# Kernel tuning notes

Hardware: AMD Instinct MI355X
Metric: run time of the kernel (lower is better)

Reference implementation:

```python
import jax, jax.numpy as jnp
import numpy as np

HIDDEN = 2048
HEADS = 16
HEAD_DIM = HIDDEN // HEADS
LATENT = 512
B, T = 2, 2048


def setup_inputs() -> dict:
    key = jax.random.key(0)
    ks = jax.random.split(key, 12)
    s = lambda fan_in: 1.0 / np.sqrt(fan_in)
    x = jax.random.normal(ks[0], (B, T, HIDDEN), dtype=jnp.float32)
    Wq = jax.random.uniform(ks[1], (HIDDEN, HIDDEN), jnp.float32, -s(HIDDEN), s(HIDDEN))
    bq = jax.random.uniform(ks[2], (HIDDEN,), jnp.float32, -s(HIDDEN), s(HIDDEN))
    Wl = jax.random.uniform(ks[3], (HIDDEN, LATENT), jnp.float32, -s(HIDDEN), s(HIDDEN))
    bl = jax.random.uniform(ks[4], (LATENT,), jnp.float32, -s(HIDDEN), s(HIDDEN))
    # per-head back-projections stacked along head axis: [H, latent, head_dim]
    Wk = jax.random.uniform(ks[5], (HEADS, LATENT, HEAD_DIM), jnp.float32, -s(LATENT), s(LATENT))
    bk = jax.random.uniform(ks[6], (HEADS, HEAD_DIM), jnp.float32, -s(LATENT), s(LATENT))
    Wv = jax.random.uniform(ks[7], (HEADS, LATENT, HEAD_DIM), jnp.float32, -s(LATENT), s(LATENT))
    bv = jax.random.uniform(ks[8], (HEADS, HEAD_DIM), jnp.float32, -s(LATENT), s(LATENT))
    Wo = jax.random.uniform(ks[9], (HIDDEN, HIDDEN), jnp.float32, -s(HIDDEN), s(HIDDEN))
    bo = jax.random.uniform(ks[10], (HIDDEN,), jnp.float32, -s(HIDDEN), s(HIDDEN))
    return {"x": x, "Wq": Wq, "bq": bq, "Wl": Wl, "bl": bl,
            "Wk": Wk, "bk": bk, "Wv": Wv, "bv": bv, "Wo": Wo, "bo": bo}


def reference(x, Wq, bq, Wl, bl, Wk, bk, Wv, bv, Wo, bo):
    Bc, Tc, _ = x.shape
    # Q projection, split into heads: [B, H, T, Dh]
    q = (x @ Wq + bq).reshape(Bc, Tc, HEADS, HEAD_DIM).transpose(0, 2, 1, 3)
    # shared low-rank latent KV (cache=None -> just new tokens): [B, T, L]
    latent = x @ Wl + bl
    # per-head back-projections fused as one grouped matmul: [B, H, T, Dh]
    k = jnp.einsum('btl,hld->bhtd', latent, Wk) + bk[None, :, None, :]
    v = jnp.einsum('btl,hld->bhtd', latent, Wv) + bv[None, :, None, :]
    # full (non-causal) attention, matching the original module
    scores = jnp.einsum('bhqd,bhkd->bhqk', q, k) / np.sqrt(HEAD_DIM).astype(jnp.float32)
    probs = jax.nn.softmax(scores, axis=-1)
    attn = jnp.einsum('bhqk,bhkd->bhqd', probs, v)
    attn = attn.transpose(0, 2, 1, 3).reshape(Bc, Tc, HIDDEN)
    return attn @ Wo + bo
```

## Files before the change

kernel.cpp:

```cpp
#include <hip/hip_runtime.h>
#include <hip/hip_bf16.h>
#include <cstdint>

#define SEQ     2048
#define NHID    2048
#define NLAT    512
#define NHEAD   16
#define DHEAD   128
#define NBATCH  2
#define NROWS   (NBATCH*SEQ)

typedef unsigned short u16;
typedef __attribute__((ext_vector_type(8))) short short8;
typedef __attribute__((ext_vector_type(4))) float f32x4;

#define MFMA16 __builtin_amdgcn_mfma_f32_16x16x32_bf16

#define QSCALE 0.12751743f

#if __has_builtin(__builtin_amdgcn_exp2f)
#define EXP2(x) __builtin_amdgcn_exp2f(x)
#else
#define EXP2(x) __expf((x) * 0.6931471805599453f)
#endif

__device__ __forceinline__ u16 f2b(float f) {
    uint32_t u = __float_as_uint(f);
    uint32_t r = (u + 0x7fffu + ((u >> 16) & 1u)) >> 16;
    return (u16)r;
}

__device__ __forceinline__ uint32_t cvt_pk_bf16(float a, float b) {
    uint32_t r;
    asm("v_cvt_pk_bf16_f32 %0, %1, %2" : "=v"(r) : "v"(a), "v"(b));
    return r;
}

__device__ __forceinline__ void async16(const u16* g, u16* l) {
    __builtin_amdgcn_global_load_lds(
        (const __attribute__((address_space(1))) unsigned int*)g,
        (__attribute__((address_space(3))) unsigned int*)l, 16, 0, 0);
}

__device__ __forceinline__ void stage_lds(const u16* __restrict__ src, size_t strideE,
                                          u16* lds, int wave, int lane,
                                          int log2cpr, int xmask, int xshift,
                                          int reps, int nlanes) {
    const int cmask = (1 << log2cpr) - 1;
    for (int rep = 0; rep < reps; ++rep) {
        int cbase = rep * nlanes + wave * 64;
        int ci = cbase + lane;
        int row = ci >> log2cpr;
        int sc = ci & cmask;
        int dchunk = sc ^ ((row >> xshift) & xmask);
        const u16* g = src + (size_t)row * strideE + dchunk * 8;
        async16(g, lds + (size_t)cbase * 8);
    }
}

__global__ __launch_bounds__(256) void prep(const float* __restrict__ x,
                                            const float* __restrict__ Wq,
                                            const float* __restrict__ Wl,
                                            const float* __restrict__ Wk,
                                            const float* __restrict__ Wv,
                                            const float* __restrict__ Wo,
                                            u16* __restrict__ xb,
                                            u16* __restrict__ WqlT,
                                            u16* __restrict__ WkvT,
                                            u16* __restrict__ WoT) {
    const int t = blockIdx.x, tid = threadIdx.x;
    if (t < 8192) {
        int i = t * 256 + tid;
        float4 v = ((const float4*)x)[i];
        unsigned int lo = (unsigned int)f2b(v.x) | ((unsigned int)f2b(v.y) << 16);
        unsigned int hi = (unsigned int)f2b(v.z) | ((unsigned int)f2b(v.w) << 16);
        ((uint2*)xb)[i] = make_uint2(lo, hi);
        return;
    }
    __shared__ float tile[32][33];
    const float* src; u16* dst; int R, C, tY, tX;
    if (t < 12288)      { int tt = t - 8192;  src = Wq; dst = WqlT;           R = 2048; C = 2048; tY = tt >> 6; tX = tt & 63; }
    else if (t < 13312) { int tt = t - 12288; src = Wl; dst = WqlT + 4194304; R = 2048; C = 512;  tY = tt >> 4; tX = tt & 15; }
    else if (t < 14336) { int tt = t - 13312; int hh = tt >> 6; tt &= 63;
                          src = Wk + hh * 65536; dst = WkvT + hh * 65536;     R = 512;  C = 128;  tY = tt >> 2; tX = tt & 3; }
    else if (t < 15360) { int tt = t - 14336; int hh = tt >> 6; tt &= 63;
                          src = Wv + hh * 65536; dst = WkvT + 1048576 + hh * 65536;
                                                                              R = 512;  C = 128;  tY = tt >> 2; tX = tt & 3; }
    else                { int tt = t - 15360; src = Wo; dst = WoT;            R = 2048; C = 2048; tY = tt >> 6; tX = tt & 63; }
    const int tx = tid & 31, ty = tid >> 5;
    const int r0 = tY * 32, c0 = tX * 32;
    #pragma unroll
    for (int i = 0; i < 32; i += 8)
        tile[ty + i][tx] = src[(size_t)(r0 + ty + i) * C + c0 + tx];
    __syncthreads();
    #pragma unroll
    for (int i = 0; i < 32; i += 8)
        dst[(size_t)(c0 + ty + i) * R + r0 + tx] = f2b(tile[tx][ty + i]);
}

template<int STORE>
__global__ __launch_bounds__(256) void gemm_bt(const u16* __restrict__ A,
                                               const u16* __restrict__ Bt,
                                               const float* __restrict__ bias1,
                                               const float* __restrict__ bias2,
                                               void* __restrict__ C1,
                                               void* __restrict__ C2,
                                               int M, int N, int K) {
    __shared__ __align__(16) u16 As[2][128 * 32];
    __shared__ __align__(16) u16 Bs[2][128 * 32];
    const int tid = threadIdx.x, wave = tid >> 6, lane = tid & 63;
    const int quad = lane >> 4, m16 = lane & 15;
    const int m0 = blockIdx.y * 128, n0 = blockIdx.x * 128;
    const int wr = wave >> 1, wc = wave & 1;
    const int swz = (quad ^ ((m16 >> 1) & 3)) * 8;
    const u16* Ab = A + (size_t)m0 * K;
    const u16* Bb = Bt + (size_t)n0 * K;
    const int KI = K >> 5;

    stage_lds(Ab, K, As[0], wave, lane, 2, 3, 1, 2, 256);
    stage_lds(Bb, K, Bs[0], wave, lane, 2, 3, 1, 2, 256);

    f32x4 acc[4][4] = {};
    for (int it = 0; it < KI; ++it) {
        const int cur = it & 1;
        __syncthreads();
        if (it + 1 < KI) {
            stage_lds(Ab + (it + 1) * 32, K, As[cur ^ 1], wave, lane, 2, 3, 1, 2, 256);
            stage_lds(Bb + (it + 1) * 32, K, Bs[cur ^ 1], wave, lane, 2, 3, 1, 2, 256);
        }
        short8 af[4], bfr[4];
        #pragma unroll
        for (int i = 0; i < 4; i++)
            af[i] = *(const short8*)&As[cur][(wr * 64 + i * 16 + m16) * 32 + swz];
        #pragma unroll
        for (int j = 0; j < 4; j++)
            bfr[j] = *(const short8*)&Bs[cur][(wc * 64 + j * 16 + m16) * 32 + swz];
        #pragma unroll
        for (int i = 0; i < 4; i++)
            #pragma unroll
            for (int j = 0; j < 4; j++)
                acc[i][j] = MFMA16(af[i], bfr[j], acc[i][j], 0, 0, 0);
    }
    const bool second = (n0 >= 2048);
    #pragma unroll
    for (int j = 0; j < 4; j++) {
        int n = n0 + wc * 64 + j * 16 + m16;
        float bv;
        if constexpr (STORE == 2) bv = bias1[n];
        else bv = second ? bias2[n - 2048] : bias1[n];
        #pragma unroll
        for (int i = 0; i < 4; i++) {
            int mrow = m0 + wr * 64 + i * 16 + quad * 4;
            if constexpr (STORE == 4) {
                if (second) {
                    int n2 = n - 2048;
                    ushort4 pk;
                    pk.x = f2b(acc[i][j][0] + bv);
                    pk.y = f2b(acc[i][j][1] + bv);
                    pk.z = f2b(acc[i][j][2] + bv);
                    pk.w = f2b(acc[i][j][3] + bv);
                    *(ushort4*)&((u16*)C2)[((size_t)((m0 >> 11) * 2048 + n2)) * 2048 +
                                           (mrow & 2047)] = pk;
                    continue;
                }
            }
            #pragma unroll
            for (int r = 0; r < 4; r++) {
                float v = acc[i][j][r] + bv;
                int m = mrow + r;
                if constexpr (STORE == 2)
                    ((float*)C1)[(size_t)m * N + n] = v;
                else if constexpr (STORE == 3) {
                    if (!second) ((u16*)C1)[(size_t)m * 2048 + n] = f2b(v * QSCALE);
                    else         ((u16*)C2)[(size_t)m * 512 + (n - 2048)] = f2b(v);
                } else {
                    ((u16*)C1)[(size_t)m * 2048 + n] = f2b(v);
                }
            }
        }
    }
}

__global__ __launch_bounds__(256, 2) void attn_fused(const u16* __restrict__ Q,
                                                     const u16* __restrict__ Kf,
                                                     const u16* __restrict__ Vt,
                                                     u16* __restrict__ Ob) {
    __shared__ __align__(16) u16 Kt[2][64 * 128];
    __shared__ __align__(16) u16 Vtile[2][128 * 64];
    __shared__ __align__(16) u16 Ps[4][32 * 64];
    const int tid = threadIdx.x, wave = tid >> 6, lane = tid & 63;
    const int quad = lane >> 4, m16 = lane & 15;
    const int bh = blockIdx.y, b = bh >> 4, h = bh & 15;
    const int q0 = blockIdx.x * 128;
    const size_t grow = (size_t)b * SEQ;
    const u16* Kbase = Kf + grow * NHID + h * DHEAD;
    const u16* Vbase = Vt + (grow + h * DHEAD) * SEQ;

    const u16* qsrc = Q + (grow + q0) * NHID + h * DHEAD;
    stage_lds(qsrc, NHID, Kt[0], wave, lane, 4, 15, 0, 4, 256);
    stage_lds(qsrc + (size_t)64 * NHID, NHID, Kt[1], wave, lane, 4, 15, 0, 4, 256);
    __syncthreads();
    short8 qf[2][4];
    {
        const u16* qbuf = Kt[wave >> 1];
        int rbase = (wave & 1) * 32;
        #pragma unroll
        for (int i = 0; i < 2; i++)
            #pragma unroll
            for (int c = 0; c < 4; c++)
                qf[i][c] = *(const short8*)&qbuf[(rbase + i * 16 + m16) * 128 +
                                                (((c * 4 + quad) ^ m16)) * 8];
    }
    __syncthreads();

    stage_lds(Kbase, NHID, Kt[0], wave, lane, 4, 15, 0, 4, 256);
    stage_lds(Vbase, SEQ, Vtile[0], wave, lane, 3, 7, 0, 4, 256);

    f32x4 o[2][8] = {};
    float lsum[2][4] = {};

    for (int it = 0; it < SEQ / 64; ++it) {
        const int cur = it & 1;
        __syncthreads();
        if (it + 1 < SEQ / 64) {
            stage_lds(Kbase + (size_t)(it + 1) * 64 * NHID, NHID, Kt[cur ^ 1],
                      wave, lane, 4, 15, 0, 4, 256);
            stage_lds(Vbase + (it + 1) * 64, SEQ, Vtile[cur ^ 1],
                      wave, lane, 3, 7, 0, 4, 256);
        }
        const u16* kt = Kt[cur];
        const u16* vt = Vtile[cur];

        f32x4 s[2][4] = {};
        __builtin_amdgcn_s_setprio(1);
        #pragma unroll
        for (int c = 0; c < 4; c++)
            #pragma unroll
            for (int j = 0; j < 4; j++) {
                short8 kb = *(const short8*)&kt[(j * 16 + m16) * 128 +
                                               (((c * 4 + quad) ^ m16)) * 8];
                s[0][j] = MFMA16(qf[0][c], kb, s[0][j], 0, 0, 0);
                s[1][j] = MFMA16(qf[1][c], kb, s[1][j], 0, 0, 0);
            }
        __builtin_amdgcn_s_setprio(0);

        u16* pw = Ps[wave];
        #pragma unroll
        for (int i = 0; i < 2; i++)
            #pragma unroll
            for (int r = 0; r < 4; r++) {
                int rowl = i * 16 + quad * 4 + r;
                float p0 = EXP2(s[i][0][r]);
                float p1 = EXP2(s[i][1][r]);
                float p2 = EXP2(s[i][2][r]);
                float p3 = EXP2(s[i][3][r]);
                lsum[i][r] += (p0 + p1) + (p2 + p3);
                uint32_t pk01 = cvt_pk_bf16(p0, p1);
                uint32_t pk23 = cvt_pk_bf16(p2, p3);
                const int x = rowl & 7;
                u16* base = pw + rowl * 64 + (m16 & 7);
                const int hb = m16 >> 3;
                base[((0 + hb) ^ x) * 8] = (u16)pk01;
                base[((2 + hb) ^ x) * 8] = (u16)(pk01 >> 16);
                base[((4 + hb) ^ x) * 8] = (u16)pk23;
                base[((6 + hb) ^ x) * 8] = (u16)(pk23 >> 16);
            }

        __builtin_amdgcn_s_setprio(1);
        #pragma unroll
        for (int c2 = 0; c2 < 2; c2++) {
            short8 pa[2];
            #pragma unroll
            for (int i = 0; i < 2; i++)
                pa[i] = *(const short8*)&pw[(i * 16 + m16) * 64 +
                                            (((c2 * 4 + quad) ^ (m16 & 7))) * 8];
            #pragma unroll
            for (int jd = 0; jd < 8; jd++) {
                short8 vb = *(const short8*)&vt[(jd * 16 + m16) * 64 +
                                               (((c2 * 4 + quad) ^ (m16 & 7))) * 8];
                o[0][jd] = MFMA16(pa[0], vb, o[0][jd], 0, 0, 0);
                o[1][jd] = MFMA16(pa[1], vb, o[1][jd], 0, 0, 0);
            }
        }
        __builtin_amdgcn_s_setprio(0);
    }

    #pragma unroll
    for (int i = 0; i < 2; i++) {
        float inv[4];
        #pragma unroll
        for (int r = 0; r < 4; r++) {
            float v = lsum[i][r];
            #pragma unroll
            for (int off = 1; off < 16; off <<= 1)
                v += __shfl_xor(v, off);
            inv[r] = 1.f / v;
        }
        #pragma unroll
        for (int jd = 0; jd < 8; jd++)
            #pragma unroll
            for (int r = 0; r < 4; r++) {
                int t = q0 + wave * 32 + i * 16 + quad * 4 + r;
                int d = jd * 16 + m16;
                Ob[(grow + t) * NHID + h * DHEAD + d] = f2b(o[i][jd][r] * inv[r]);
            }
    }
}

extern "C" void kernel_launch(void* const* d_in, const int* in_sizes, int n_in,
                              void* d_out, int out_size, void* d_ws, size_t ws_size,
                              hipStream_t stream) {
    const float* x  = (const float*)d_in[0];
    const float* Wq = (const float*)d_in[1];
    const float* bq = (const float*)d_in[2];
    const float* Wl = (const float*)d_in[3];
    const float* bl = (const float*)d_in[4];
    const float* Wk = (const float*)d_in[5];
    const float* bk = (const float*)d_in[6];
    const float* Wv = (const float*)d_in[7];
    const float* bv = (const float*)d_in[8];
    const float* Wo = (const float*)d_in[9];
    const float* bo = (const float*)d_in[10];
    float* out = (float*)d_out;

    u16* w = (u16*)d_ws;
    u16* xb    = w;
    u16* WqlT  = xb    + 8388608;
    u16* WkvT  = WqlT  + 5242880;
    u16* WoT   = WkvT  + 2097152;
    u16* qb    = WoT   + 4194304;
    u16* kb    = qb    + 8388608;
    u16* vt    = kb    + 8388608;
    u16* lat   = vt    + 8388608;
    u16* attnb = xb;

    prep<<<19456, 256, 0, stream>>>(x, Wq, Wl, Wk, Wv, Wo, xb, WqlT, WkvT, WoT);

    gemm_bt<3><<<dim3(20, 32), 256, 0, stream>>>(xb, WqlT, bq, bl, qb, lat,
                                                 NROWS, 2560, 2048);
    gemm_bt<4><<<dim3(32, 32), 256, 0, stream>>>(lat, WkvT, bk, bv, kb, vt,
                                                 NROWS, 4096, 512);

    attn_fused<<<dim3(16, 32), 256, 0, stream>>>(qb, kb, vt, attnb);

    gemm_bt<2><<<dim3(16, 32), 256, 0, stream>>>(attnb, WoT, bo, nullptr, out, nullptr,
                                                 NROWS, 2048, 2048);
}
```

Measured before the change: 343.9 us.

## Keep softmax probabilities in registers via transposed QK MFMA and permlane swaps

Swaps the MFMA operand order for QK^T so each lane holds score columns for one query row. The bf16 probabilities can then be assembled into PV A-operands with permlane32 swaps instead of a round-trip through LDS. To make the k-index order match, the V-transpose store in the projection GEMM permutes bits 2 and 3 of the sequence index. This removes the per-wave P shared-memory buffer and its stores, loads and bank traffic, and simplifies the row-sum reduction, at the cost of a coupled layout change across two kernels.

```diff
diff --git a/kernel.cpp b/kernel.cpp
--- a/kernel.cpp
+++ b/kernel.cpp
@@ -154,13 +154,14 @@
             if constexpr (STORE == 4) {
                 if (second) {
                     int n2 = n - 2048;
-                    ushort4 pk;
-                    pk.x = f2b(acc[i][j][0] + bv);
-                    pk.y = f2b(acc[i][j][1] + bv);
-                    pk.z = f2b(acc[i][j][2] + bv);
-                    pk.w = f2b(acc[i][j][3] + bv);
-                    *(ushort4*)&((u16*)C2)[((size_t)((m0 >> 11) * 2048 + n2)) * 2048 +
-                                           (mrow & 2047)] = pk;
+                    ushort4 pkv;
+                    pkv.x = f2b(acc[i][j][0] + bv);
+                    pkv.y = f2b(acc[i][j][1] + bv);
+                    pkv.z = f2b(acc[i][j][2] + bv);
+                    pkv.w = f2b(acc[i][j][3] + bv);
+                    int c = mrow & 2047;
+                    c = (c & ~12) | ((c & 4) << 1) | ((c & 8) >> 1);
+                    *(ushort4*)&((u16*)C2)[((size_t)((m0 >> 11) * 2048 + n2)) * 2048 + c] = pkv;
                     continue;
                 }
             }
@@ -187,7 +188,6 @@
                                                      u16* __restrict__ Ob) {
     __shared__ __align__(16) u16 Kt[2][64 * 128];
     __shared__ __align__(16) u16 Vtile[2][128 * 64];
-    __shared__ __align__(16) u16 Ps[4][32 * 64];
     const int tid = threadIdx.x, wave = tid >> 6, lane = tid & 63;
     const int quad = lane >> 4, m16 = lane & 15;
     const int bh = blockIdx.y, b = bh >> 4, h = bh & 15;
@@ -217,7 +217,7 @@
     stage_lds(Vbase, SEQ, Vtile[0], wave, lane, 3, 7, 0, 4, 256);
 
     f32x4 o[2][8] = {};
-    float lsum[2][4] = {};
+    float lsum[2] = {};
 
     for (int it = 0; it < SEQ / 64; ++it) {
         const int cur = it & 1;
@@ -239,41 +239,56 @@
             for (int j = 0; j < 4; j++) {
                 short8 kb = *(const short8*)&kt[(j * 16 + m16) * 128 +
                                                (((c * 4 + quad) ^ m16)) * 8];
-                s[0][j] = MFMA16(qf[0][c], kb, s[0][j], 0, 0, 0);
-                s[1][j] = MFMA16(qf[1][c], kb, s[1][j], 0, 0, 0);
+                s[0][j] = MFMA16(kb, qf[0][c], s[0][j], 0, 0, 0);
+                s[1][j] = MFMA16(kb, qf[1][c], s[1][j], 0, 0, 0);
             }
         __builtin_amdgcn_s_setprio(0);
 
-        u16* pw = Ps[wave];
-        #pragma unroll
-        for (int i = 0; i < 2; i++)
-            #pragma unroll
-            for (int r = 0; r < 4; r++) {
-                int rowl = i * 16 + quad * 4 + r;
-                float p0 = EXP2(s[i][0][r]);
-                float p1 = EXP2(s[i][1][r]);
-                float p2 = EXP2(s[i][2][r]);
-                float p3 = EXP2(s[i][3][r]);
-                lsum[i][r] += (p0 + p1) + (p2 + p3);
-                uint32_t pk01 = cvt_pk_bf16(p0, p1);
-                uint32_t pk23 = cvt_pk_bf16(p2, p3);
-                const int x = rowl & 7;
-                u16* base = pw + rowl * 64 + (m16 & 7);
-                const int hb = m16 >> 3;
-                base[((0 + hb) ^ x) * 8] = (u16)pk01;
-                base[((2 + hb) ^ x) * 8] = (u16)(pk01 >> 16);
-                base[((4 + hb) ^ x) * 8] = (u16)pk23;
-                base[((6 + hb) ^ x) * 8] = (u16)(pk23 >> 16);
-            }
+        uint32_t pk[2][4][2];
+        #pragma unroll
+        for (int i = 0; i < 2; i++) {
+            float rs = 0.f;
+            #pragma unroll
+            for (int j = 0; j < 4; j++) {
+                float p0 = EXP2(s[i][j][0]);
+                float p1 = EXP2(s[i][j][1]);
+                float p2 = EXP2(s[i][j][2]);
+                float p3 = EXP2(s[i][j][3]);
+                rs += (p0 + p1) + (p2 + p3);
+                pk[i][j][0] = cvt_pk_bf16(p0, p1);
+                pk[i][j][1] = cvt_pk_bf16(p2, p3);
+            }
+            lsum[i] += rs;
+        }
 
         __builtin_amdgcn_s_setprio(1);
         #pragma unroll
         for (int c2 = 0; c2 < 2; c2++) {
             short8 pa[2];
             #pragma unroll
-            for (int i = 0; i < 2; i++)
-                pa[i] = *(const short8*)&pw[(i * 16 + m16) * 64 +
-                                            (((c2 * 4 + quad) ^ (m16 & 7))) * 8];
+            for (int i = 0; i < 2; i++) {
+                union { uint32_t u[4]; short8 s8; } pu;
+#if __has_builtin(__builtin_amdgcn_permlane32_swap)
+                auto r0 = __builtin_amdgcn_permlane32_swap(pk[i][2 * c2][0],
+                                                           pk[i][2 * c2 + 1][0],
+                                                           false, false);
+                auto r1 = __builtin_amdgcn_permlane32_swap(pk[i][2 * c2][1],
+                                                           pk[i][2 * c2 + 1][1],
+                                                           false, false);
+                pu.u[0] = r0[0]; pu.u[1] = r1[0]; pu.u[2] = r0[1]; pu.u[3] = r1[1];
+#else
+                uint32_t jl0 = pk[i][2 * c2][0],     jl1 = pk[i][2 * c2][1];
+                uint32_t jh0 = pk[i][2 * c2 + 1][0], jh1 = pk[i][2 * c2 + 1][1];
+                uint32_t sl0 = __shfl_xor(jl0, 32), sl1 = __shfl_xor(jl1, 32);
+                uint32_t sh0 = __shfl_xor(jh0, 32), sh1 = __shfl_xor(jh1, 32);
+                const bool low = lane < 32;
+                pu.u[0] = low ? jl0 : sh0;
+                pu.u[1] = low ? jl1 : sh1;
+                pu.u[2] = low ? sl0 : jh0;
+                pu.u[3] = low ? sl1 : jh1;
+#endif
+                pa[i] = pu.s8;
+            }
             #pragma unroll
             for (int jd = 0; jd < 8; jd++) {
                 short8 vb = *(const short8*)&vt[(jd * 16 + m16) * 64 +
@@ -287,15 +302,17 @@
 
     #pragma unroll
     for (int i = 0; i < 2; i++) {
+        float v = lsum[i];
+        v += __shfl_xor(v, 16);
+        v += __shfl_xor(v, 32);
+        lsum[i] = v;
+    }
+    #pragma unroll
+    for (int i = 0; i < 2; i++) {
         float inv[4];
         #pragma unroll
-        for (int r = 0; r < 4; r++) {
-            float v = lsum[i][r];
-            #pragma unroll
-            for (int off = 1; off < 16; off <<= 1)
-                v += __shfl_xor(v, off);
-            inv[r] = 1.f / v;
-        }
+        for (int r = 0; r < 4; r++)
+            inv[r] = 1.f / __shfl(lsum[i], quad * 4 + r);
         #pragma unroll
         for (int jd = 0; jd < 8; jd++)
             #pragma unroll
```

New measurement: 340.0 us. Within noise of the previous version (-1.1%).
